# Optimization experiments

Measured on AMD Instinct MI355X. Metric: run time of the kernel, lower is better.

Reference implementation:

```python
import jax, jax.numpy as jnp
import numpy as np

N = 50000      # nodes
E = 800000     # edges (before self-loops)
IN = 128
HID = 128
OUT = 64
L = 8          # num_layers
ALPHA = 0.1
THETA = 0.5
BN_EPS = 1e-5


def setup_inputs() -> dict:
    key = jax.random.key(0)
    ks = jax.random.split(key, 8)
    x = jax.random.normal(ks[0], (N, IN), dtype=jnp.float32)
    edge_index = jax.random.randint(ks[1], (2, E), 0, N, dtype=jnp.int32)
    # nn.Linear default init: U(-1/sqrt(fan_in), 1/sqrt(fan_in))
    s0 = 1.0 / np.sqrt(IN)
    lin0_w = jax.random.uniform(ks[2], (HID, IN), jnp.float32, -s0, s0)
    lin0_b = jax.random.uniform(ks[3], (HID,), jnp.float32, -s0, s0)
    s1 = 1.0 / np.sqrt(HID)
    lin1_w = jax.random.uniform(ks[4], (OUT, HID), jnp.float32, -s1, s1)
    lin1_b = jax.random.uniform(ks[5], (OUT,), jnp.float32, -s1, s1)
    # GCN2Conv weight1: glorot, shape [HID, HID], applied as h @ W
    g = np.sqrt(6.0 / (HID + HID))
    conv_w = jax.random.uniform(ks[6], (L, HID, HID), jnp.float32, -g, g)
    bn_gamma = jnp.ones((L, HID), jnp.float32)
    bn_beta = jnp.zeros((L, HID), jnp.float32)
    return {"x": x, "edge_index": edge_index, "lin0_w": lin0_w, "lin0_b": lin0_b,
            "lin1_w": lin1_w, "lin1_b": lin1_b, "conv_w": conv_w,
            "bn_gamma": bn_gamma, "bn_beta": bn_beta}


def _gcn_norm(edge_index):
    """PyG gcn_norm with add_self_loops=True, improved=False."""
    loops = jnp.arange(N, dtype=edge_index.dtype)
    src = jnp.concatenate([edge_index[0], loops])
    dst = jnp.concatenate([edge_index[1], loops])
    w = jnp.ones(src.shape[0], jnp.float32)
    deg = jax.ops.segment_sum(w, dst, num_segments=N)
    dinv = jnp.where(deg > 0, jax.lax.rsqrt(jnp.maximum(deg, 1e-12)), 0.0)
    norm = dinv[src] * w * dinv[dst]
    return src, dst, norm


def reference(x, edge_index, lin0_w, lin0_b, lin1_w, lin1_b, conv_w, bn_gamma, bn_beta):
    src, dst, norm = _gcn_norm(edge_index)
    # input projection (dropout is identity in eval/reference mode)
    h = jax.nn.relu(x @ lin0_w.T + lin0_b)
    h0 = h
    for i in range(L):
        # sparse adjacency propagation: out[dst] += norm * h[src]
        agg = jax.ops.segment_sum(norm[:, None] * h[src], dst, num_segments=N)
        # GCN2Conv with shared weights, normalize=False
        z = (1.0 - ALPHA) * agg + ALPHA * h0
        beta = float(np.log(THETA / (i + 1) + 1.0))
        z = (1.0 - beta) * z + beta * (z @ conv_w[i])
        # BatchNorm1d over nodes (batch statistics, biased variance)
        mean = z.mean(axis=0)
        var = z.var(axis=0)
        z = (z - mean) * jax.lax.rsqrt(var + BN_EPS) * bn_gamma[i] + bn_beta[i]
        h = jax.nn.relu(z)
    return h @ lin1_w.T + lin1_b
```

## Files before the change

### kernel.cpp

```cpp
#include <hip/hip_runtime.h>
#include <hip/hip_bf16.h>
#include <math.h>

#define N_NODES 50000
#define N_EDGES 800000
#define NLAYERS 8
#define ALPHA_C 0.1f
#define BN_EPS  1e-5f

typedef unsigned short u16;
typedef __attribute__((ext_vector_type(8))) short short8;
typedef __attribute__((ext_vector_type(4))) float f32x4;

static __device__ __forceinline__ u16 f2bf(float f) {
    unsigned u = __float_as_uint(f);
    unsigned r = (u + 0x7fffu + ((u >> 16) & 1u)) >> 16;
    return (u16)r;
}
static __device__ __forceinline__ float bf2f(u16 b) {
    return __uint_as_float((unsigned)b << 16);
}
static __device__ __forceinline__ float blo(unsigned w) { return __uint_as_float(w << 16); }
static __device__ __forceinline__ float bhi(unsigned w) { return __uint_as_float(w & 0xffff0000u); }

__global__ __launch_bounds__(256) void k_init(int* cnt, int* fill, float* stats) {
    int i = blockIdx.x * 256 + threadIdx.x;
    if (i < N_NODES) { cnt[i] = 0; fill[i] = 0; }
    if (i < NLAYERS * 256) stats[i] = 0.0f;
}

__global__ __launch_bounds__(256) void k_count(const int* __restrict__ dst, int* cnt) {
    int e = blockIdx.x * 256 + threadIdx.x;
    if (e < N_EDGES) atomicAdd(&cnt[dst[e]], 1);
}

__global__ __launch_bounds__(256) void k_dinv(const int* __restrict__ cnt, float* __restrict__ dinv) {
    int i = blockIdx.x * 256 + threadIdx.x;
    if (i < N_NODES) dinv[i] = rsqrtf((float)(cnt[i] + 1));
}

__global__ __launch_bounds__(128) void k_perm_local(const int* __restrict__ cnt, int* __restrict__ perm) {
    __shared__ int keys[128];
    int t = threadIdx.x;
    int base = blockIdx.x * 128;
    int i = base + t;
    int k = (i < N_NODES) ? cnt[i] : 0x7fffffff;
    keys[t] = k;
    __syncthreads();
    if (i < N_NODES) {
        int r = 0;
#pragma unroll 8
        for (int j = 0; j < 128; ++j) {
            int kj = keys[j];
            r += (kj < k) || (kj == k && j < t);
        }
        perm[base + r] = i;
    }
}

__global__ __launch_bounds__(1024) void k_scan_local(const int* __restrict__ cnt,
                                                     int* __restrict__ rowptr, int* __restrict__ bsum) {
    __shared__ int tmp[1024];
    int t = threadIdx.x;
    int i = blockIdx.x * 1024 + t;
    int v = (i < N_NODES) ? cnt[i] : 0;
    tmp[t] = v;
    __syncthreads();
    for (int off = 1; off < 1024; off <<= 1) {
        int y = (t >= off) ? tmp[t - off] : 0;
        __syncthreads();
        tmp[t] += y;
        __syncthreads();
    }
    if (i < N_NODES) rowptr[i] = tmp[t] - v;
    if (t == 1023) bsum[blockIdx.x] = tmp[t];
}

__global__ void k_scan_top(int* bsum) {
    __shared__ int tmp[64];
    int t = threadIdx.x;
    int v = (t < 49) ? bsum[t] : 0;
    tmp[t] = v;
    __syncthreads();
    for (int off = 1; off < 64; off <<= 1) {
        int y = (t >= off) ? tmp[t - off] : 0;
        __syncthreads();
        tmp[t] += y;
        __syncthreads();
    }
    if (t < 49) bsum[t] = tmp[t] - v;
}

__global__ __launch_bounds__(256) void k_scan_add(int* __restrict__ rowptr, const int* __restrict__ bsum) {
    int i = blockIdx.x * 256 + threadIdx.x;
    if (i < N_NODES) rowptr[i] += bsum[i >> 10];
    if (i == 0) rowptr[N_NODES] = N_EDGES;
}

__global__ __launch_bounds__(256) void k_scatter(const int* __restrict__ src, const int* __restrict__ dst,
                                                 const int* __restrict__ rowptr, int* fill,
                                                 u16* __restrict__ ssrc) {
    int e = blockIdx.x * 256 + threadIdx.x;
    if (e < N_EDGES) {
        int d = dst[e];
        int pos = rowptr[d] + atomicAdd(&fill[d], 1);
        ssrc[pos] = (u16)src[e];
    }
}

__global__ __launch_bounds__(256) void k_convw(const float* __restrict__ conv_w,
                                               const float* __restrict__ lin0_w,
                                               const float* __restrict__ lin1_w,
                                               u16* __restrict__ wtb) {
    int t = blockIdx.x * 256 + threadIdx.x;
    if (t < 131072) {
        int j = (t >> 7) & 127, k = t & 127;
        int i = t >> 14;
        float v = conv_w[(i << 14) + (k << 7) + j];
        wtb[(t & ~127) | (k ^ ((j & 7) << 3))] = f2bf(v);
    } else if (t < 131072 + 16384) {
        int u = t - 131072;
        int j = u >> 7, k = u & 127;
        wtb[131072 + ((u & ~127) | (k ^ ((j & 7) << 3)))] = f2bf(lin0_w[u]);
    } else if (t < 131072 + 16384 + 8192) {
        int u = t - 147456;
        int j = u >> 7, k = u & 127;
        wtb[147456 + ((u & ~127) | (k ^ ((j & 7) << 3)))] = f2bf(lin1_w[u]);
    }
}

__global__ __launch_bounds__(256) void k_convx(const float* __restrict__ x, u16* __restrict__ xb) {
    size_t i = ((size_t)blockIdx.x * 256 + threadIdx.x) * 4;
    int row = (int)(i >> 7), j = (int)(i & 127);
    float4 v = *(const float4*)(x + i);
    uint2 o;
    o.x = (unsigned)f2bf(v.x) | ((unsigned)f2bf(v.y) << 16);
    o.y = (unsigned)f2bf(v.z) | ((unsigned)f2bf(v.w) << 16);
    *(uint2*)(xb + ((size_t)(j >> 4) * N_NODES + row) * 16 + (j & 15)) = o;
}

template<int NT, int MODE>
__global__ __launch_bounds__(256) void k_gemm_mfma(const u16* __restrict__ A,
                                                   const u16* __restrict__ Wg,
                                                   const float* __restrict__ bias,
                                                   float* __restrict__ Zf,
                                                   u16* __restrict__ h0b,
                                                   u16* __restrict__ hbp,
                                                   float* __restrict__ outF,
                                                   float* __restrict__ stats,
                                                   const float* __restrict__ dinv,
                                                   float beta_c, int M) {
    __shared__ u16 Ws[NT * 16 * 128];
    __shared__ float sstat[256];
    int tid = threadIdx.x;

    {
        const float4* srcv = (const float4*)Wg;
        float4* dstv = (float4*)Ws;
#pragma unroll
        for (int i = 0; i < NT; ++i) dstv[tid + i * 256] = srcv[tid + i * 256];
    }
    if (MODE == 1) sstat[tid] = 0.f;

    int wave = tid >> 6, lane = tid & 63;
    int r0 = blockIdx.x * 64 + wave * 16;
    int kg = lane >> 4;
    int cl = lane & 15;

    int arow = r0 + cl;
    int acl = arow < M ? arow : M - 1;
    short8 afrag[4];
#pragma unroll
    for (int kk = 0; kk < 4; ++kk) {
        int s = kk * 2 + (kg >> 1);
        afrag[kk] = *(const short8*)(A + ((size_t)s * N_NODES + acl) * 16 + (kg & 1) * 8);
    }

    __syncthreads();

    f32x4 acc[NT];
#pragma unroll
    for (int nt = 0; nt < NT; ++nt) {
        acc[nt] = (f32x4){0.f, 0.f, 0.f, 0.f};
        int j = nt * 16 + cl;
        const u16* wrow = Ws + j * 128;
        int sw = (j & 7) << 3;
#pragma unroll
        for (int kk = 0; kk < 4; ++kk) {
            short8 b = *(const short8*)(wrow + ((kk * 32 + kg * 8) ^ sw));
            acc[nt] = __builtin_amdgcn_mfma_f32_16x16x32_bf16(afrag[kk], b, acc[nt], 0, 0, 0);
        }
    }

    int rbase = r0 + kg * 4;
    float dvr[4];
    if (MODE != 1) {
#pragma unroll
        for (int reg = 0; reg < 4; ++reg) {
            int row = rbase + reg;
            dvr[reg] = (row < M) ? dinv[row] : 1.f;
        }
    }

#pragma unroll
    for (int nt = 0; nt < NT; ++nt) {
        int j = nt * 16 + cl;
        float s = 0.f, ss = 0.f;
#pragma unroll
        for (int reg = 0; reg < 4; ++reg) {
            int row = rbase + reg;
            if (row >= M) continue;
            float v = acc[nt][reg];
            size_t idx = ((size_t)nt * N_NODES + row) * 16 + cl;
            if (MODE == 0) {
                v = fmaxf(v + bias[j], 0.f);
                h0b[idx] = f2bf(v);
                hbp[idx] = f2bf(v * dvr[reg]);
            } else if (MODE == 1) {
                float zin = bf2f(A[idx]);
                v = (1.0f - beta_c) * zin + beta_c * v;
                Zf[idx] = v;
                s += v;
                ss = fmaf(v, v, ss);
            } else {
                outF[(size_t)row * (NT * 16) + j] = v / dvr[reg] + bias[j];
            }
        }
        if (MODE == 1) {
            s  += __shfl_xor(s, 16);  s  += __shfl_xor(s, 32);
            ss += __shfl_xor(ss, 16); ss += __shfl_xor(ss, 32);
            if (kg == 0) {
                atomicAdd(&sstat[j], s);
                atomicAdd(&sstat[128 + j], ss);
            }
        }
    }
    if (MODE == 1) {
        __syncthreads();
        atomicAdd(&stats[tid], sstat[tid]);
    }
}

__global__ __launch_bounds__(256) void k_aggregate(const u16* __restrict__ hbp, const u16* __restrict__ h0b,
                                                   const int* __restrict__ rowptr, const u16* __restrict__ ssrc,
                                                   const float* __restrict__ dinv, const int* __restrict__ perm,
                                                   u16* __restrict__ Zb) {
    int slice = blockIdx.x & 7;
    int wave = threadIdx.x >> 6, lane = threadIdx.x & 63;
    int rg = lane >> 1, hf = lane & 1;
    int idx = (blockIdx.x >> 3) * 128 + wave * 32 + rg;
    if (idx >= N_NODES) return;
    int v = perm[idx];
    const u16* hs = hbp + (size_t)slice * ((size_t)N_NODES * 16);
    int beg = rowptr[v], end = rowptr[v + 1];

    float a0, a1, a2, a3, a4, a5, a6, a7;
    {
        uint4 u = *(const uint4*)(hs + (size_t)v * 16 + hf * 8);
        a0 = blo(u.x); a1 = bhi(u.x); a2 = blo(u.y); a3 = bhi(u.y);
        a4 = blo(u.z); a5 = bhi(u.z); a6 = blo(u.w); a7 = bhi(u.w);
    }
    int p = beg;
    for (; p + 8 <= end; p += 8) {
        uint4 u0 = *(const uint4*)(hs + (size_t)ssrc[p + 0] * 16 + hf * 8);
        uint4 u1 = *(const uint4*)(hs + (size_t)ssrc[p + 1] * 16 + hf * 8);
        uint4 u2 = *(const uint4*)(hs + (size_t)ssrc[p + 2] * 16 + hf * 8);
        uint4 u3 = *(const uint4*)(hs + (size_t)ssrc[p + 3] * 16 + hf * 8);
        uint4 u4 = *(const uint4*)(hs + (size_t)ssrc[p + 4] * 16 + hf * 8);
        uint4 u5 = *(const uint4*)(hs + (size_t)ssrc[p + 5] * 16 + hf * 8);
        uint4 u6 = *(const uint4*)(hs + (size_t)ssrc[p + 6] * 16 + hf * 8);
        uint4 u7 = *(const uint4*)(hs + (size_t)ssrc[p + 7] * 16 + hf * 8);
        a0 += blo(u0.x); a1 += bhi(u0.x); a2 += blo(u0.y); a3 += bhi(u0.y);
        a4 += blo(u0.z); a5 += bhi(u0.z); a6 += blo(u0.w); a7 += bhi(u0.w);
        a0 += blo(u1.x); a1 += bhi(u1.x); a2 += blo(u1.y); a3 += bhi(u1.y);
        a4 += blo(u1.z); a5 += bhi(u1.z); a6 += blo(u1.w); a7 += bhi(u1.w);
        a0 += blo(u2.x); a1 += bhi(u2.x); a2 += blo(u2.y); a3 += bhi(u2.y);
        a4 += blo(u2.z); a5 += bhi(u2.z); a6 += blo(u2.w); a7 += bhi(u2.w);
        a0 += blo(u3.x); a1 += bhi(u3.x); a2 += blo(u3.y); a3 += bhi(u3.y);
        a4 += blo(u3.z); a5 += bhi(u3.z); a6 += blo(u3.w); a7 += bhi(u3.w);
        a0 += blo(u4.x); a1 += bhi(u4.x); a2 += blo(u4.y); a3 += bhi(u4.y);
        a4 += blo(u4.z); a5 += bhi(u4.z); a6 += blo(u4.w); a7 += bhi(u4.w);
        a0 += blo(u5.x); a1 += bhi(u5.x); a2 += blo(u5.y); a3 += bhi(u5.y);
        a4 += blo(u5.z); a5 += bhi(u5.z); a6 += blo(u5.w); a7 += bhi(u5.w);
        a0 += blo(u6.x); a1 += bhi(u6.x); a2 += blo(u6.y); a3 += bhi(u6.y);
        a4 += blo(u6.z); a5 += bhi(u6.z); a6 += blo(u6.w); a7 += bhi(u6.w);
        a0 += blo(u7.x); a1 += bhi(u7.x); a2 += blo(u7.y); a3 += bhi(u7.y);
        a4 += blo(u7.z); a5 += bhi(u7.z); a6 += blo(u7.w); a7 += bhi(u7.w);
    }
    for (; p < end; ++p) {
        uint4 u = *(const uint4*)(hs + (size_t)ssrc[p] * 16 + hf * 8);
        a0 += blo(u.x); a1 += bhi(u.x); a2 += blo(u.y); a3 += bhi(u.y);
        a4 += blo(u.z); a5 += bhi(u.z); a6 += blo(u.w); a7 += bhi(u.w);
    }

    float dv = dinv[v] * (1.0f - ALPHA_C);
    size_t oidx = ((size_t)slice * N_NODES + v) * 16 + hf * 8;
    uint4 uh = *(const uint4*)(h0b + oidx);
    float z0 = dv * a0 + ALPHA_C * blo(uh.x);
    float z1 = dv * a1 + ALPHA_C * bhi(uh.x);
    float z2 = dv * a2 + ALPHA_C * blo(uh.y);
    float z3 = dv * a3 + ALPHA_C * bhi(uh.y);
    float z4 = dv * a4 + ALPHA_C * blo(uh.z);
    float z5 = dv * a5 + ALPHA_C * bhi(uh.z);
    float z6 = dv * a6 + ALPHA_C * blo(uh.w);
    float z7 = dv * a7 + ALPHA_C * bhi(uh.w);
    uint4 o;
    o.x = (unsigned)f2bf(z0) | ((unsigned)f2bf(z1) << 16);
    o.y = (unsigned)f2bf(z2) | ((unsigned)f2bf(z3) << 16);
    o.z = (unsigned)f2bf(z4) | ((unsigned)f2bf(z5) << 16);
    o.w = (unsigned)f2bf(z6) | ((unsigned)f2bf(z7) << 16);
    *(uint4*)(Zb + oidx) = o;
}

__global__ __launch_bounds__(256) void k_bn_relu(const float* __restrict__ Zf, const float* __restrict__ stats,
                                                 const float* __restrict__ gamma, const float* __restrict__ betap,
                                                 const float* __restrict__ dinv, u16* __restrict__ hbp) {
    __shared__ float ssc[128], ssh[128];
    int t = threadIdx.x;
    if (t < 128) {
        float mean = stats[t] * (1.0f / N_NODES);
        float var = stats[128 + t] * (1.0f / N_NODES) - mean * mean;
        float istd = rsqrtf(var + BN_EPS);
        float sc = gamma[t] * istd;
        ssc[t] = sc;
        ssh[t] = betap[t] - mean * sc;
    }
    __syncthreads();
    int e4 = blockIdx.x * 256 + t;
    if (e4 >= N_NODES * 32) return;
    int slice = e4 / (N_NODES * 4);
    int rem = e4 - slice * (N_NODES * 4);
    int row = rem >> 2;
    int j0 = slice * 16 + (rem & 3) * 4;
    float dv = dinv[row];
    float4 z = *(const float4*)(Zf + (size_t)e4 * 4);
    float r0 = fmaxf(fmaf(z.x, ssc[j0 + 0], ssh[j0 + 0]), 0.f) * dv;
    float r1 = fmaxf(fmaf(z.y, ssc[j0 + 1], ssh[j0 + 1]), 0.f) * dv;
    float r2 = fmaxf(fmaf(z.z, ssc[j0 + 2], ssh[j0 + 2]), 0.f) * dv;
    float r3 = fmaxf(fmaf(z.w, ssc[j0 + 3], ssh[j0 + 3]), 0.f) * dv;
    uint2 o;
    o.x = (unsigned)f2bf(r0) | ((unsigned)f2bf(r1) << 16);
    o.y = (unsigned)f2bf(r2) | ((unsigned)f2bf(r3) << 16);
    *(uint2*)(hbp + (size_t)e4 * 4) = o;
}


extern "C" void kernel_launch(void* const* d_in, const int* in_sizes, int n_in,
                              void* d_out, int out_size, void* d_ws, size_t ws_size,
                              hipStream_t stream) {
    const float* x      = (const float*)d_in[0];
    const int*   ei     = (const int*)d_in[1];
    const float* lin0_w = (const float*)d_in[2];
    const float* lin0_b = (const float*)d_in[3];
    const float* lin1_w = (const float*)d_in[4];
    const float* lin1_b = (const float*)d_in[5];
    const float* conv_w = (const float*)d_in[6];
    const float* bn_g   = (const float*)d_in[7];
    const float* bn_b   = (const float*)d_in[8];
    const int* e_src = ei;
    const int* e_dst = ei + N_EDGES;

    char* p = (char*)d_ws;
    auto alloc = [&](size_t bytes) -> void* {
        void* r = (void*)p;
        p += (bytes + 255) & ~(size_t)255;
        return r;
    };
    int*   cnt    = (int*)alloc((size_t)N_NODES * 4);
    int*   rowptr = (int*)alloc((size_t)(N_NODES + 1) * 4);
    int*   fill   = (int*)alloc((size_t)N_NODES * 4);
    float* dinv   = (float*)alloc((size_t)N_NODES * 4);
    u16*   ssrc   = (u16*)alloc((size_t)N_EDGES * 2);
    int*   bsum   = (int*)alloc(64 * 4);
    int*   perm   = (int*)alloc((size_t)N_NODES * 4);
    u16*   h0b    = (u16*)alloc((size_t)N_NODES * 128 * 2);
    float* Zf     = (float*)alloc((size_t)N_NODES * 128 * 4);
    u16*   Zb     = (u16*)alloc((size_t)N_NODES * 128 * 2);
    u16*   hbp    = (u16*)alloc((size_t)N_NODES * 128 * 2);
    u16*   wtb    = (u16*)alloc((size_t)(131072 + 16384 + 8192) * 2);
    float* stats  = (float*)alloc((size_t)NLAYERS * 256 * 4);

    const int nblk = (N_NODES + 255) / 256;
    const int eblk = (N_EDGES + 255) / 256;
    const int gblk = (N_NODES + 63) / 64;
    const int vblk = N_NODES * 128 / 4 / 256;
    const int ablk = ((N_NODES + 127) / 128) * 8;
    const int pblk = (N_NODES + 127) / 128;
    const int bnblk = (N_NODES * 32 + 255) / 256;

    k_init<<<nblk, 256, 0, stream>>>(cnt, fill, stats);
    k_count<<<eblk, 256, 0, stream>>>(e_dst, cnt);
    k_dinv<<<nblk, 256, 0, stream>>>(cnt, dinv);
    k_perm_local<<<pblk, 128, 0, stream>>>(cnt, perm);
    k_scan_local<<<49, 1024, 0, stream>>>(cnt, rowptr, bsum);
    k_scan_top<<<1, 64, 0, stream>>>(bsum);
    k_scan_add<<<196, 256, 0, stream>>>(rowptr, bsum);
    k_scatter<<<eblk, 256, 0, stream>>>(e_src, e_dst, rowptr, fill, ssrc);
    k_convw<<<(131072 + 16384 + 8192 + 255) / 256, 256, 0, stream>>>(conv_w, lin0_w, lin1_w, wtb);
    k_convx<<<vblk, 256, 0, stream>>>(x, Zb);

    k_gemm_mfma<8, 0><<<gblk, 256, 0, stream>>>(Zb, wtb + 131072, lin0_b, nullptr, h0b, hbp, nullptr, nullptr, dinv, 0.f, N_NODES);

    for (int i = 0; i < NLAYERS; ++i) {
        k_aggregate<<<ablk, 256, 0, stream>>>(hbp, h0b, rowptr, ssrc, dinv, perm, Zb);
        float beta = (float)log(0.5 / (double)(i + 1) + 1.0);
        k_gemm_mfma<8, 1><<<gblk, 256, 0, stream>>>(Zb, wtb + (size_t)i * 16384, nullptr, Zf, nullptr, nullptr, nullptr, stats + (size_t)i * 256, nullptr, beta, N_NODES);
        k_bn_relu<<<bnblk, 256, 0, stream>>>(Zf, stats + (size_t)i * 256, bn_g + i * 128, bn_b + i * 128, dinv, hbp);
    }

    k_gemm_mfma<4, 2><<<gblk, 256, 0, stream>>>(hbp, wtb + 147456, lin1_b, nullptr, nullptr, nullptr, (float*)d_out, nullptr, dinv, 0.f, N_NODES);
}
```

Measured before the change: 850.5 us.

## Pad CSR rows to multiples of 8 with dummy node, widen feature slices, fuse setup kernels

Each CSR row is padded to a multiple of 8 entries. The padding points at a zeroed dummy node N, so the aggregation loop drops its scalar tail and loads 8 source indices at once as a uint4. Feature slices grow from 16 to 32 bf16 columns (4 slices instead of 8), with a row stride of NP. Aggregation now uses 4 lanes per row with 64 rows per block. The setup kernels (count, weight/x conversion, ssrc fill, dinv/perm/scan) are merged into fewer launches. This costs some extra gather work on padded entries and a larger ssrc buffer.

```diff
diff --git a/kernel.cpp b/kernel.cpp
--- a/kernel.cpp
+++ b/kernel.cpp
@@ -3,7 +3,9 @@
 #include <math.h>
 
 #define N_NODES 50000
+#define NP      (N_NODES + 1)
 #define N_EDGES 800000
+#define SSRC_CAP (N_EDGES + 8 * N_NODES)
 #define NLAYERS 8
 #define ALPHA_C 0.1f
 #define BN_EPS  1e-5f
@@ -23,48 +25,90 @@
 static __device__ __forceinline__ float blo(unsigned w) { return __uint_as_float(w << 16); }
 static __device__ __forceinline__ float bhi(unsigned w) { return __uint_as_float(w & 0xffff0000u); }
 
-__global__ __launch_bounds__(256) void k_init(int* cnt, int* fill, float* stats) {
+__global__ __launch_bounds__(256) void k_init(int* cnt, int* fill, float* stats, u16* hbp) {
     int i = blockIdx.x * 256 + threadIdx.x;
     if (i < N_NODES) { cnt[i] = 0; fill[i] = 0; }
     if (i < NLAYERS * 256) stats[i] = 0.0f;
-}
-
-__global__ __launch_bounds__(256) void k_count(const int* __restrict__ dst, int* cnt) {
-    int e = blockIdx.x * 256 + threadIdx.x;
-    if (e < N_EDGES) atomicAdd(&cnt[dst[e]], 1);
-}
-
-__global__ __launch_bounds__(256) void k_dinv(const int* __restrict__ cnt, float* __restrict__ dinv) {
-    int i = blockIdx.x * 256 + threadIdx.x;
-    if (i < N_NODES) dinv[i] = rsqrtf((float)(cnt[i] + 1));
-}
-
-__global__ __launch_bounds__(128) void k_perm_local(const int* __restrict__ cnt, int* __restrict__ perm) {
-    __shared__ int keys[128];
+    if (i < 128) {
+        int s = i >> 5, c = i & 31;
+        hbp[((size_t)s * NP + N_NODES) * 32 + c] = 0;
+    }
+}
+
+#define CB_COUNT 3125
+#define CB_CONVW 608
+#define CB_CONVX 6250
+#define CB_FILL  587
+
+__global__ __launch_bounds__(256) void k_countprep(const int* __restrict__ dst, int* cnt,
+                                                   const float* __restrict__ conv_w,
+                                                   const float* __restrict__ lin0_w,
+                                                   const float* __restrict__ lin1_w,
+                                                   u16* __restrict__ wtb,
+                                                   const float* __restrict__ x, u16* __restrict__ xb,
+                                                   u16* __restrict__ ssrc) {
+    int b = blockIdx.x;
+    if (b < CB_COUNT) {
+        int e = b * 256 + threadIdx.x;
+        if (e < N_EDGES) atomicAdd(&cnt[dst[e]], 1);
+    } else if (b < CB_COUNT + CB_CONVW) {
+        int t = (b - CB_COUNT) * 256 + threadIdx.x;
+        if (t < 131072) {
+            int j = (t >> 7) & 127, k = t & 127;
+            int i = t >> 14;
+            float v = conv_w[(i << 14) + (k << 7) + j];
+            wtb[(t & ~127) | (k ^ ((j & 7) << 3))] = f2bf(v);
+        } else if (t < 131072 + 16384) {
+            int u = t - 131072;
+            int j = u >> 7, k = u & 127;
+            wtb[131072 + ((u & ~127) | (k ^ ((j & 7) << 3)))] = f2bf(lin0_w[u]);
+        } else if (t < 131072 + 16384 + 8192) {
+            int u = t - 147456;
+            int j = u >> 7, k = u & 127;
+            wtb[147456 + ((u & ~127) | (k ^ ((j & 7) << 3)))] = f2bf(lin1_w[u]);
+        }
+    } else if (b < CB_COUNT + CB_CONVW + CB_CONVX) {
+        size_t i = ((size_t)(b - CB_COUNT - CB_CONVW) * 256 + threadIdx.x) * 4;
+        int row = (int)(i >> 7), j = (int)(i & 127);
+        float4 v = *(const float4*)(x + i);
+        uint2 o;
+        o.x = (unsigned)f2bf(v.x) | ((unsigned)f2bf(v.y) << 16);
+        o.y = (unsigned)f2bf(v.z) | ((unsigned)f2bf(v.w) << 16);
+        *(uint2*)(xb + ((size_t)(j >> 5) * NP + row) * 32 + (j & 31)) = o;
+    } else {
+        size_t q = ((size_t)(b - CB_COUNT - CB_CONVW - CB_CONVX) * 256 + threadIdx.x);
+        unsigned pat = (unsigned)N_NODES | ((unsigned)N_NODES << 16);
+        if (q * 8 < SSRC_CAP) {
+            uint4 o = make_uint4(pat, pat, pat, pat);
+            *(uint4*)(ssrc + q * 8) = o;
+        }
+    }
+}
+
+__global__ __launch_bounds__(1024) void k_graphA(const int* __restrict__ cnt, float* __restrict__ dinv,
+                                                 int* __restrict__ perm,
+                                                 int* __restrict__ rowptr, int* __restrict__ bsum) {
+    __shared__ int tmp[1024];
     int t = threadIdx.x;
-    int base = blockIdx.x * 128;
-    int i = base + t;
-    int k = (i < N_NODES) ? cnt[i] : 0x7fffffff;
-    keys[t] = k;
-    __syncthreads();
-    if (i < N_NODES) {
+    int i = blockIdx.x * 1024 + t;
+    int deg = (i < N_NODES) ? cnt[i] : 0;
+    if (i < N_NODES) dinv[i] = rsqrtf((float)(deg + 1));
+    tmp[t] = (i < N_NODES) ? deg : 0x7fffffff;
+    __syncthreads();
+    {
+        int g = t >> 7, tl = t & 127;
+        int k = tmp[t];
         int r = 0;
 #pragma unroll 8
         for (int j = 0; j < 128; ++j) {
-            int kj = keys[j];
-            r += (kj < k) || (kj == k && j < t);
-        }
-        perm[base + r] = i;
-    }
-}
-
-__global__ __launch_bounds__(1024) void k_scan_local(const int* __restrict__ cnt,
-                                                     int* __restrict__ rowptr, int* __restrict__ bsum) {
-    __shared__ int tmp[1024];
-    int t = threadIdx.x;
-    int i = blockIdx.x * 1024 + t;
-    int v = (i < N_NODES) ? cnt[i] : 0;
-    tmp[t] = v;
+            int kj = tmp[(g << 7) + j];
+            r += (kj < k) || (kj == k && j < tl);
+        }
+        if (i < N_NODES) perm[blockIdx.x * 1024 + (g << 7) + r] = i;
+    }
+    __syncthreads();
+    int vpad = (i < N_NODES) ? ((deg + 7) & ~7) : 0;
+    tmp[t] = vpad;
     __syncthreads();
     for (int off = 1; off < 1024; off <<= 1) {
         int y = (t >= off) ? tmp[t - off] : 0;
@@ -72,7 +116,7 @@
         tmp[t] += y;
         __syncthreads();
     }
-    if (i < N_NODES) rowptr[i] = tmp[t] - v;
+    if (i < N_NODES) rowptr[i] = tmp[t] - vpad;
     if (t == 1023) bsum[blockIdx.x] = tmp[t];
 }
 
@@ -89,12 +133,13 @@
         __syncthreads();
     }
     if (t < 49) bsum[t] = tmp[t] - v;
+    if (t == 48) bsum[63] = tmp[48];
 }
 
 __global__ __launch_bounds__(256) void k_scan_add(int* __restrict__ rowptr, const int* __restrict__ bsum) {
     int i = blockIdx.x * 256 + threadIdx.x;
     if (i < N_NODES) rowptr[i] += bsum[i >> 10];
-    if (i == 0) rowptr[N_NODES] = N_EDGES;
+    if (i == 0) rowptr[N_NODES] = bsum[63];
 }
 
 __global__ __launch_bounds__(256) void k_scatter(const int* __restrict__ src, const int* __restrict__ dst,
@@ -106,37 +151,6 @@
         int pos = rowptr[d] + atomicAdd(&fill[d], 1);
         ssrc[pos] = (u16)src[e];
     }
-}
-
-__global__ __launch_bounds__(256) void k_convw(const float* __restrict__ conv_w,
-                                               const float* __restrict__ lin0_w,
-                                               const float* __restrict__ lin1_w,
-                                               u16* __restrict__ wtb) {
-    int t = blockIdx.x * 256 + threadIdx.x;
-    if (t < 131072) {
-        int j = (t >> 7) & 127, k = t & 127;
-        int i = t >> 14;
-        float v = conv_w[(i << 14) + (k << 7) + j];
-        wtb[(t & ~127) | (k ^ ((j & 7) << 3))] = f2bf(v);
-    } else if (t < 131072 + 16384) {
-        int u = t - 131072;
-        int j = u >> 7, k = u & 127;
-        wtb[131072 + ((u & ~127) | (k ^ ((j & 7) << 3)))] = f2bf(lin0_w[u]);
-    } else if (t < 131072 + 16384 + 8192) {
-        int u = t - 147456;
-        int j = u >> 7, k = u & 127;
-        wtb[147456 + ((u & ~127) | (k ^ ((j & 7) << 3)))] = f2bf(lin1_w[u]);
-    }
-}
-
-__global__ __launch_bounds__(256) void k_convx(const float* __restrict__ x, u16* __restrict__ xb) {
-    size_t i = ((size_t)blockIdx.x * 256 + threadIdx.x) * 4;
-    int row = (int)(i >> 7), j = (int)(i & 127);
-    float4 v = *(const float4*)(x + i);
-    uint2 o;
-    o.x = (unsigned)f2bf(v.x) | ((unsigned)f2bf(v.y) << 16);
-    o.y = (unsigned)f2bf(v.z) | ((unsigned)f2bf(v.w) << 16);
-    *(uint2*)(xb + ((size_t)(j >> 4) * N_NODES + row) * 16 + (j & 15)) = o;
 }
 
 template<int NT, int MODE>
@@ -171,10 +185,8 @@
     int acl = arow < M ? arow : M - 1;
     short8 afrag[4];
 #pragma unroll
-    for (int kk = 0; kk < 4; ++kk) {
-        int s = kk * 2 + (kg >> 1);
-        afrag[kk] = *(const short8*)(A + ((size_t)s * N_NODES + acl) * 16 + (kg & 1) * 8);
-    }
+    for (int kk = 0; kk < 4; ++kk)
+        afrag[kk] = *(const short8*)(A + ((size_t)kk * NP + acl) * 32 + kg * 8);
 
     __syncthreads();
 
@@ -211,7 +223,7 @@
             int row = rbase + reg;
             if (row >= M) continue;
             float v = acc[nt][reg];
-            size_t idx = ((size_t)nt * N_NODES + row) * 16 + cl;
+            size_t idx = ((size_t)(nt >> 1) * NP + row) * 32 + (nt & 1) * 16 + cl;
             if (MODE == 0) {
                 v = fmaxf(v + bias[j], 0.f);
                 h0b[idx] = f2bf(v);
@@ -245,31 +257,39 @@
                                                    const int* __restrict__ rowptr, const u16* __restrict__ ssrc,
                                                    const float* __restrict__ dinv, const int* __restrict__ perm,
                                                    u16* __restrict__ Zb) {
-    int slice = blockIdx.x & 7;
+    int slice = blockIdx.x & 3;
     int wave = threadIdx.x >> 6, lane = threadIdx.x & 63;
-    int rg = lane >> 1, hf = lane & 1;
-    int idx = (blockIdx.x >> 3) * 128 + wave * 32 + rg;
+    int rg = lane >> 2, hf = lane & 3;
+    int idx = (blockIdx.x >> 2) * 64 + wave * 16 + rg;
     if (idx >= N_NODES) return;
     int v = perm[idx];
-    const u16* hs = hbp + (size_t)slice * ((size_t)N_NODES * 16);
-    int beg = rowptr[v], end = rowptr[v + 1];
+    const u16* hs = hbp + (size_t)slice * NP * 32;
+    int beg = rowptr[v];
+    int nit = (rowptr[v + 1] - beg) >> 3;
 
     float a0, a1, a2, a3, a4, a5, a6, a7;
     {
-        uint4 u = *(const uint4*)(hs + (size_t)v * 16 + hf * 8);
+        uint4 u = *(const uint4*)(hs + (size_t)v * 32 + hf * 8);
         a0 = blo(u.x); a1 = bhi(u.x); a2 = blo(u.y); a3 = bhi(u.y);
         a4 = blo(u.z); a5 = bhi(u.z); a6 = blo(u.w); a7 = bhi(u.w);
     }
-    int p = beg;
-    for (; p + 8 <= end; p += 8) {
-        uint4 u0 = *(const uint4*)(hs + (size_t)ssrc[p + 0] * 16 + hf * 8);
-        uint4 u1 = *(const uint4*)(hs + (size_t)ssrc[p + 1] * 16 + hf * 8);
-        uint4 u2 = *(const uint4*)(hs + (size_t)ssrc[p + 2] * 16 + hf * 8);
-        uint4 u3 = *(const uint4*)(hs + (size_t)ssrc[p + 3] * 16 + hf * 8);
-        uint4 u4 = *(const uint4*)(hs + (size_t)ssrc[p + 4] * 16 + hf * 8);
-        uint4 u5 = *(const uint4*)(hs + (size_t)ssrc[p + 5] * 16 + hf * 8);
-        uint4 u6 = *(const uint4*)(hs + (size_t)ssrc[p + 6] * 16 + hf * 8);
-        uint4 u7 = *(const uint4*)(hs + (size_t)ssrc[p + 7] * 16 + hf * 8);
+    const uint4* sv = (const uint4*)(ssrc + beg);
+    uint4 S;
+    if (nit > 0) S = sv[0];
+    for (int it = 0; it < nit; ++it) {
+        uint4 Sn = (it + 1 < nit) ? sv[it + 1] : S;
+        int s0 = S.x & 0xffff, s1 = S.x >> 16;
+        int s2 = S.y & 0xffff, s3 = S.y >> 16;
+        int s4 = S.z & 0xffff, s5 = S.z >> 16;
+        int s6 = S.w & 0xffff, s7 = S.w >> 16;
+        uint4 u0 = *(const uint4*)(hs + (size_t)s0 * 32 + hf * 8);
+        uint4 u1 = *(const uint4*)(hs + (size_t)s1 * 32 + hf * 8);
+        uint4 u2 = *(const uint4*)(hs + (size_t)s2 * 32 + hf * 8);
+        uint4 u3 = *(const uint4*)(hs + (size_t)s3 * 32 + hf * 8);
+        uint4 u4 = *(const uint4*)(hs + (size_t)s4 * 32 + hf * 8);
+        uint4 u5 = *(const uint4*)(hs + (size_t)s5 * 32 + hf * 8);
+        uint4 u6 = *(const uint4*)(hs + (size_t)s6 * 32 + hf * 8);
+        uint4 u7 = *(const uint4*)(hs + (size_t)s7 * 32 + hf * 8);
         a0 += blo(u0.x); a1 += bhi(u0.x); a2 += blo(u0.y); a3 += bhi(u0.y);
         a4 += blo(u0.z); a5 += bhi(u0.z); a6 += blo(u0.w); a7 += bhi(u0.w);
         a0 += blo(u1.x); a1 += bhi(u1.x); a2 += blo(u1.y); a3 += bhi(u1.y);
@@ -286,15 +306,11 @@
         a4 += blo(u6.z); a5 += bhi(u6.z); a6 += blo(u6.w); a7 += bhi(u6.w);
         a0 += blo(u7.x); a1 += bhi(u7.x); a2 += blo(u7.y); a3 += bhi(u7.y);
         a4 += blo(u7.z); a5 += bhi(u7.z); a6 += blo(u7.w); a7 += bhi(u7.w);
-    }
-    for (; p < end; ++p) {
-        uint4 u = *(const uint4*)(hs + (size_t)ssrc[p] * 16 + hf * 8);
-        a0 += blo(u.x); a1 += bhi(u.x); a2 += blo(u.y); a3 += bhi(u.y);
-        a4 += blo(u.z); a5 += bhi(u.z); a6 += blo(u.w); a7 += bhi(u.w);
+        S = Sn;
     }
 
     float dv = dinv[v] * (1.0f - ALPHA_C);
-    size_t oidx = ((size_t)slice * N_NODES + v) * 16 + hf * 8;
+    size_t oidx = ((size_t)slice * NP + v) * 32 + hf * 8;
     uint4 uh = *(const uint4*)(h0b + oidx);
     float z0 = dv * a0 + ALPHA_C * blo(uh.x);
     float z1 = dv * a1 + ALPHA_C * bhi(uh.x);
@@ -328,12 +344,14 @@
     __syncthreads();
     int e4 = blockIdx.x * 256 + t;
     if (e4 >= N_NODES * 32) return;
-    int slice = e4 / (N_NODES * 4);
-    int rem = e4 - slice * (N_NODES * 4);
-    int row = rem >> 2;
-    int j0 = slice * 16 + (rem & 3) * 4;
+    int slice = e4 / (N_NODES * 8);
+    int rem = e4 - slice * (N_NODES * 8);
+    int row = rem >> 3;
+    int q = rem & 7;
+    size_t addr = ((size_t)slice * NP + row) * 32 + q * 4;
+    int j0 = slice * 32 + q * 4;
     float dv = dinv[row];
-    float4 z = *(const float4*)(Zf + (size_t)e4 * 4);
+    float4 z = *(const float4*)(Zf + addr);
     float r0 = fmaxf(fmaf(z.x, ssc[j0 + 0], ssh[j0 + 0]), 0.f) * dv;
     float r1 = fmaxf(fmaf(z.y, ssc[j0 + 1], ssh[j0 + 1]), 0.f) * dv;
     float r2 = fmaxf(fmaf(z.z, ssc[j0 + 2], ssh[j0 + 2]), 0.f) * dv;
@@ -341,7 +359,7 @@
     uint2 o;
     o.x = (unsigned)f2bf(r0) | ((unsigned)f2bf(r1) << 16);
     o.y = (unsigned)f2bf(r2) | ((unsigned)f2bf(r3) << 16);
-    *(uint2*)(hbp + (size_t)e4 * 4) = o;
+    *(uint2*)(hbp + addr) = o;
 }
 
 
@@ -370,34 +388,29 @@
     int*   rowptr = (int*)alloc((size_t)(N_NODES + 1) * 4);
     int*   fill   = (int*)alloc((size_t)N_NODES * 4);
     float* dinv   = (float*)alloc((size_t)N_NODES * 4);
-    u16*   ssrc   = (u16*)alloc((size_t)N_EDGES * 2);
+    u16*   ssrc   = (u16*)alloc((size_t)SSRC_CAP * 2);
     int*   bsum   = (int*)alloc(64 * 4);
     int*   perm   = (int*)alloc((size_t)N_NODES * 4);
-    u16*   h0b    = (u16*)alloc((size_t)N_NODES * 128 * 2);
-    float* Zf     = (float*)alloc((size_t)N_NODES * 128 * 4);
-    u16*   Zb     = (u16*)alloc((size_t)N_NODES * 128 * 2);
-    u16*   hbp    = (u16*)alloc((size_t)N_NODES * 128 * 2);
+    u16*   h0b    = (u16*)alloc((size_t)4 * NP * 32 * 2);
+    float* Zf     = (float*)alloc((size_t)4 * NP * 32 * 4);
+    u16*   Zb     = (u16*)alloc((size_t)4 * NP * 32 * 2);
+    u16*   hbp    = (u16*)alloc((size_t)4 * NP * 32 * 2);
     u16*   wtb    = (u16*)alloc((size_t)(131072 + 16384 + 8192) * 2);
     float* stats  = (float*)alloc((size_t)NLAYERS * 256 * 4);
 
     const int nblk = (N_NODES + 255) / 256;
     const int eblk = (N_EDGES + 255) / 256;
     const int gblk = (N_NODES + 63) / 64;
-    const int vblk = N_NODES * 128 / 4 / 256;
-    const int ablk = ((N_NODES + 127) / 128) * 8;
-    const int pblk = (N_NODES + 127) / 128;
+    const int ablk = ((N_NODES + 63) / 64) * 4;
     const int bnblk = (N_NODES * 32 + 255) / 256;
-
-    k_init<<<nblk, 256, 0, stream>>>(cnt, fill, stats);
-    k_count<<<eblk, 256, 0, stream>>>(e_dst, cnt);
-    k_dinv<<<nblk, 256, 0, stream>>>(cnt, dinv);
-    k_perm_local<<<pblk, 128, 0, stream>>>(cnt, perm);
-    k_scan_local<<<49, 1024, 0, stream>>>(cnt, rowptr, bsum);
+    const int cpblk = CB_COUNT + CB_CONVW + CB_CONVX + CB_FILL;
+
+    k_init<<<nblk, 256, 0, stream>>>(cnt, fill, stats, hbp);
+    k_countprep<<<cpblk, 256, 0, stream>>>(e_dst, cnt, conv_w, lin0_w, lin1_w, wtb, x, Zb, ssrc);
+    k_graphA<<<49, 1024, 0, stream>>>(cnt, dinv, perm, rowptr, bsum);
     k_scan_top<<<1, 64, 0, stream>>>(bsum);
     k_scan_add<<<196, 256, 0, stream>>>(rowptr, bsum);
     k_scatter<<<eblk, 256, 0, stream>>>(e_src, e_dst, rowptr, fill, ssrc);
-    k_convw<<<(131072 + 16384 + 8192 + 255) / 256, 256, 0, stream>>>(conv_w, lin0_w, lin1_w, wtb);
-    k_convx<<<vblk, 256, 0, stream>>>(x, Zb);
 
     k_gemm_mfma<8, 0><<<gblk, 256, 0, stream>>>(Zb, wtb + 131072, lin0_b, nullptr, h0b, hbp, nullptr, nullptr, dinv, 0.f, N_NODES);
 
```

Result: faster. 822.5 us (-3.3%).
